# Performance work log

Measured on AMD Instinct MI355X. Metric: run time of the kernel, lower is better.

Reference implementation:

```python
import jax, jax.numpy as jnp
import numpy as np

N = 50000      # nodes
E = 800000     # edges
D = 128        # in = out features (required by Euler residual update)
GRID_SIZE = 5
K = 3          # spline order
GRID_LO, GRID_HI = -1.0, 1.0
EPSILON = 0.001
NUM_BASES = GRID_SIZE + K  # 8


def make_grid(in_features):
    # extended uniform grid: [in, grid_size + 2k + 1]
    h = (GRID_HI - GRID_LO) / GRID_SIZE
    g = jnp.arange(-K, GRID_SIZE + K + 1, dtype=jnp.float32) * h + GRID_LO
    return jnp.broadcast_to(g, (in_features, g.shape[0]))


def b_splines(x, grid):
    # x: [N, in]; grid: [in, g+2k+1] -> bases: [N, in, g+k] (Cox-de Boor)
    xe = x[..., None]
    bases = ((xe >= grid[:, :-1]) & (xe < grid[:, 1:])).astype(x.dtype)
    for j in range(1, K + 1):
        left = (xe - grid[:, : -(j + 1)]) / (grid[:, j:-1] - grid[:, : -(j + 1)])
        right = (grid[:, j + 1:] - xe) / (grid[:, j + 1:] - grid[:, 1:-j])
        bases = left * bases[..., :-1] + right * bases[..., 1:]
    return bases


def kan_transform(x, base_w, spline_w, grid):
    # efficient-KAN layer (scale_and_bias=False): silu base branch + spline branch
    base = jax.nn.silu(x) @ base_w.T                    # [N, out]
    sb = b_splines(x, grid)                             # [N, in, g+k]
    spl = jnp.einsum('nib,oib->no', sb, spline_w)       # [N, out]
    return base + spl


def gcn_norm_coeffs(edge_index, n):
    # A_hat symmetric normalization: deg includes self-loop (+1)
    src, dst = edge_index[0], edge_index[1]
    deg = jnp.zeros((n,), jnp.float32).at[dst].add(1.0) + 1.0
    dis = jax.lax.rsqrt(deg)
    return dis[src] * dis[dst]


def setup_inputs() -> dict:
    key = jax.random.key(0)
    ks = jax.random.split(key, 6)
    x = jax.random.uniform(ks[0], (N, D), jnp.float32) * 2.0 - 1.0  # in grid_range
    edge_index = jax.random.randint(ks[1], (2, E), 0, N, dtype=jnp.int64)
    base_w_l = jax.random.normal(ks[2], (D, D), jnp.float32) * (1.0 / np.sqrt(D))
    spline_w_l = jax.random.normal(ks[3], (D, D, NUM_BASES), jnp.float32) * 0.1
    base_w_c = jax.random.normal(ks[4], (D, D), jnp.float32) * (1.0 / np.sqrt(D))
    spline_w_c = jax.random.normal(ks[5], (D, D, NUM_BASES), jnp.float32) * 0.1
    return {"x": x, "edge_index": edge_index, "base_w_l": base_w_l,
            "spline_w_l": spline_w_l, "base_w_c": base_w_c,
            "spline_w_c": spline_w_c, "delta_t": 2}


def reference(x, edge_index, base_w_l, spline_w_l, base_w_c, spline_w_c, delta_t):
    grid = make_grid(D)
    src, dst = edge_index[0], edge_index[1]
    norm = gcn_norm_coeffs(edge_index, N)  # [E]

    def layer(h):
        # KANLayer branch on node features
        h_l = kan_transform(h, base_w_l, spline_w_l, grid)
        # KANConv branch: aggregate_first -> normalized scatter-add, then KAN
        msgs = norm[:, None] * h[src]                              # [E, D]
        agg = jax.ops.segment_sum(msgs, dst, num_segments=N)       # [N, D]
        h_c = kan_transform(agg, base_w_c, spline_w_c, grid)
        return h_l + h_c

    for _ in range(int(delta_t)):   # explicit Euler ODE steps
        x = x + EPSILON * layer(x)
    return x
```

## Files before the change

### kernel.cpp

```cpp
#include <hip/hip_runtime.h>
#include <hip/hip_bf16.h>

#define NNODES 50000
#define NEDGES 800000
#define DF 128
#define KW 1152
#define EPS 0.001f
#define NB 196

typedef __bf16 bf16x8 __attribute__((ext_vector_type(8)));
typedef __bf16 bf16x4 __attribute__((ext_vector_type(4)));
typedef float  f32x4  __attribute__((ext_vector_type(4)));
typedef unsigned long ulongx2 __attribute__((ext_vector_type(2)));

__global__ void build_wt(const float* __restrict__ bwl, const float* __restrict__ swl,
                         const float* __restrict__ bwc, const float* __restrict__ swc,
                         __bf16* __restrict__ wtf) {
    int idx = blockIdx.x * 256 + threadIdx.x;
    int j    = idx & 7;
    int lane = (idx >> 3) & 63;
    int nj   = (idx >> 9) & 7;
    int t    = idx >> 12;
    int l15 = lane & 15, q = lane >> 4;
    int bc = (t >= 36);
    int ck = bc ? t - 36 : t;
    const float* bw = bc ? bwc : bwl;
    const float* sw = bc ? swc : swl;
    int row = nj * 16 + l15;
    int k = ck * 32 + q * 8 + j;
    float v = (k < 128) ? bw[row * DF + k] : sw[row * 1024 + (k - 128)];
    wtf[idx] = (__bf16)v;
}

__global__ void cast_x(const float* __restrict__ x, __bf16* __restrict__ xb) {
    int i = blockIdx.x * 256 + threadIdx.x;
    f32x4 a = ((const f32x4*)x)[2 * i];
    f32x4 b = ((const f32x4*)x)[2 * i + 1];
    bf16x8 o;
    o[0] = (__bf16)a[0]; o[1] = (__bf16)a[1]; o[2] = (__bf16)a[2]; o[3] = (__bf16)a[3];
    o[4] = (__bf16)b[0]; o[5] = (__bf16)b[1]; o[6] = (__bf16)b[2]; o[7] = (__bf16)b[3];
    ((bf16x8*)xb)[i] = o;
}

__global__ void deg_count(const int* __restrict__ ei, int* __restrict__ deg) {
    int e = blockIdx.x * 256 + threadIdx.x;
    if (e >= NEDGES) return;
    atomicAdd(&deg[ei[NEDGES + e]], 1);
}

__global__ void scan_part(const int* __restrict__ deg, int* __restrict__ bsum) {
    __shared__ int red[256];
    int t = threadIdx.x;
    int i = blockIdx.x * 256 + t;
    red[t] = (i < NNODES) ? deg[i] : 0;
    __syncthreads();
    for (int off = 128; off > 0; off >>= 1) {
        if (t < off) red[t] += red[t + off];
        __syncthreads();
    }
    if (t == 0) bsum[blockIdx.x] = red[0];
}

__global__ void scan_bsum(const int* __restrict__ bsum, int* __restrict__ boff) {
    __shared__ int buf[256];
    int t = threadIdx.x;
    int v = (t < NB) ? bsum[t] : 0;
    buf[t] = v;
    __syncthreads();
    for (int off = 1; off < 256; off <<= 1) {
        int x = (t >= off) ? buf[t - off] : 0;
        __syncthreads();
        buf[t] += x;
        __syncthreads();
    }
    if (t <= NB) boff[t] = buf[t] - ((t < NB) ? bsum[t] : 0);
}

__global__ void scan_final(const int* __restrict__ deg, const int* __restrict__ boff,
                           int* __restrict__ rowptr) {
    __shared__ int buf[256];
    int t = threadIdx.x;
    int i = blockIdx.x * 256 + t;
    int v = (i < NNODES) ? deg[i] : 0;
    buf[t] = v;
    __syncthreads();
    for (int off = 1; off < 256; off <<= 1) {
        int x = (t >= off) ? buf[t - off] : 0;
        __syncthreads();
        buf[t] += x;
        __syncthreads();
    }
    if (i < NNODES) rowptr[i] = buf[t] - v + boff[blockIdx.x];
    if (blockIdx.x == 0 && t == 0) rowptr[NNODES] = boff[NB];
}

__global__ void fill_csr(const int* __restrict__ ei, const int* __restrict__ deg,
                         const int* __restrict__ rowptr, int* __restrict__ cnt,
                         int* __restrict__ esrc, float* __restrict__ ew) {
    int e = blockIdx.x * 256 + threadIdx.x;
    if (e >= NEDGES) return;
    int s = ei[e];
    int d = ei[NEDGES + e];
    float w = rsqrtf((float)(deg[s] + 1)) * rsqrtf((float)(deg[d] + 1));
    int p = rowptr[d] + atomicAdd(&cnt[d], 1);
    esrc[p] = s;
    ew[p] = w;
}

__global__ __launch_bounds__(256) void agg_gather(
        const int* __restrict__ rowptr, const int* __restrict__ esrc,
        const float* __restrict__ ew, const __bf16* __restrict__ hb,
        __bf16* __restrict__ aggb) {
    const int tid = blockIdx.x * 256 + threadIdx.x;
    const int n = tid >> 4;
    const int l = tid & 15;
    if (n >= NNODES) return;
    int p  = rowptr[n];
    const int pe = rowptr[n + 1];
    float acc[8] = {};
    int   cs0, cs1, cs2, cs3;
    float cw0, cw1, cw2, cw3;
    bool have = (p + 3 < pe);
    if (have) {
        cs0 = esrc[p]; cs1 = esrc[p + 1]; cs2 = esrc[p + 2]; cs3 = esrc[p + 3];
        cw0 = ew[p];   cw1 = ew[p + 1];   cw2 = ew[p + 2];   cw3 = ew[p + 3];
    }
    while (have) {
        int np = p + 4;
        bool nh = (np + 3 < pe);
        int   ns0 = 0, ns1 = 0, ns2 = 0, ns3 = 0;
        float nw0 = 0, nw1 = 0, nw2 = 0, nw3 = 0;
        if (nh) {
            ns0 = esrc[np]; ns1 = esrc[np + 1]; ns2 = esrc[np + 2]; ns3 = esrc[np + 3];
            nw0 = ew[np];   nw1 = ew[np + 1];   nw2 = ew[np + 2];   nw3 = ew[np + 3];
        }
        bf16x8 v0 = *(const bf16x8*)(hb + (size_t)cs0 * DF + l * 8);
        bf16x8 v1 = *(const bf16x8*)(hb + (size_t)cs1 * DF + l * 8);
        bf16x8 v2 = *(const bf16x8*)(hb + (size_t)cs2 * DF + l * 8);
        bf16x8 v3 = *(const bf16x8*)(hb + (size_t)cs3 * DF + l * 8);
#pragma unroll
        for (int j = 0; j < 8; ++j)
            acc[j] += cw0 * (float)v0[j] + cw1 * (float)v1[j]
                    + cw2 * (float)v2[j] + cw3 * (float)v3[j];
        p = np;
        cs0 = ns0; cs1 = ns1; cs2 = ns2; cs3 = ns3;
        cw0 = nw0; cw1 = nw1; cw2 = nw2; cw3 = nw3;
        have = nh;
    }
    for (; p < pe; ++p) {
        int   s0 = esrc[p];
        float w0 = ew[p];
        bf16x8 v0 = *(const bf16x8*)(hb + (size_t)s0 * DF + l * 8);
#pragma unroll
        for (int j = 0; j < 8; ++j) acc[j] += w0 * (float)v0[j];
    }
    bf16x8 o;
#pragma unroll
    for (int j = 0; j < 8; ++j) o[j] = (__bf16)acc[j];
    *(bf16x8*)(aggb + (size_t)n * DF + l * 8) = o;
}

__global__ __launch_bounds__(256, 3) void kan_step(
        const float* __restrict__ h,
        const __bf16* __restrict__ xb,
        const __bf16* __restrict__ aggb,
        const __bf16* __restrict__ wtf,
        float* __restrict__ out, __bf16* __restrict__ outb) {
    __shared__ __bf16 Xs[64 * 128];

    const int tid  = threadIdx.x;
    const int lane = tid & 63;
    const int w    = tid >> 6;
    const int q    = lane >> 4, l15 = lane & 15;
    const int n0   = blockIdx.x * 64;
    const int myrow = w * 16 + l15;
    const int msw   = myrow & 7;

    const int xrow = tid >> 2, xseg = tid & 3;
    const bool xok = (n0 + xrow) < NNODES;
    const size_t xgoff = (size_t)(n0 + xrow) * DF + xseg * 32;

    const __bf16* fbase = wtf + (size_t)lane * 8;

    f32x4 acc[8] = {};

    auto xs_write = [&](uint4 v0, uint4 v1, uint4 v2, uint4 v3) {
        const int gl = xrow * 16 + xseg * 4;
        const int sw = xrow & 7;
        *(uint4*)&Xs[(size_t)((gl + 0) ^ sw) * 8] = v0;
        *(uint4*)&Xs[(size_t)((gl + 1) ^ sw) * 8] = v1;
        *(uint4*)&Xs[(size_t)((gl + 2) ^ sw) * 8] = v2;
        *(uint4*)&Xs[(size_t)((gl + 3) ^ sw) * 8] = v3;
    };

    auto loadF = [&](bf16x8 (&bX)[8], int t) {
        const __bf16* fb = fbase + (size_t)t * 4096;
#pragma unroll
        for (int nj = 0; nj < 8; ++nj)
            bX[nj] = *(const bf16x8*)(fb + nj * 512);
    };

    auto spline_pack = [&](float x) -> bf16x8 {
        float f  = __builtin_fmaf(x, 2.5f, 5.5f);
        float fi = floorf(f);
        int  idx = (int)fi;
        float u  = f - fi;
        float u2 = u * u, u3 = u2 * u;
        float om = 1.0f - u;
        float Wa = u3 * (1.0f / 6.0f);
        float Wb = (((-3.0f * u + 3.0f) * u + 3.0f) * u + 1.0f) * (1.0f / 6.0f);
        float Wc = ((3.0f * u - 6.0f) * u2 + 4.0f) * (1.0f / 6.0f);
        float Wd = om * om * om * (1.0f / 6.0f);
        unsigned long p =
              (unsigned long)__builtin_bit_cast(unsigned short, (__bf16)Wd)
            | ((unsigned long)__builtin_bit_cast(unsigned short, (__bf16)Wc) << 16)
            | ((unsigned long)__builtin_bit_cast(unsigned short, (__bf16)Wb) << 32)
            | ((unsigned long)__builtin_bit_cast(unsigned short, (__bf16)Wa) << 48);
        int tt = idx - 3;
        unsigned long lo, hi;
        if (tt >= 0) {
            int s = (tt & 3) * 16;
            unsigned long sv = p << s;
            unsigned long cr = (p >> (63 - s)) >> 1;
            bool hh = tt >= 4;
            lo = hh ? 0ul : sv;
            hi = hh ? sv : cr;
            if (tt >= 8) { lo = 0; hi = 0; }
        } else {
            int s = (-tt) * 16;
            lo = (tt >= -3) ? (p >> (s & 63)) : 0ul;
            hi = 0;
        }
        ulongx2 r; r[0] = lo; r[1] = hi;
        return __builtin_bit_cast(bf16x8, r);
    };

    auto silu8 = [&](const __bf16* xs) -> bf16x8 {
        bf16x8 v = *(const bf16x8*)xs;
        bf16x8 o;
#pragma unroll
        for (int j = 0; j < 8; ++j) {
            float x = (float)v[j];
            o[j] = (__bf16)(x / (1.0f + __expf(-x)));
        }
        return o;
    };

    auto compute = [&](int t, const bf16x8 (&bF)[8]) {
        const int ck = (t >= 36) ? t - 36 : t;
        bf16x8 a;
        if (ck < 4) {
            const int g = (myrow * 16 + ck * 4 + q) ^ msw;
            a = silu8(&Xs[(size_t)g * 8]);
        } else {
            const int f = (ck - 4) * 4 + q;
            const int g = (myrow * 16 + (f >> 3)) ^ msw;
            unsigned short u0 =
                *(const unsigned short*)&Xs[(size_t)g * 8 + (f & 7)];
            a = spline_pack(__builtin_bit_cast(float, (unsigned)u0 << 16));
        }
#pragma unroll
        for (int nj = 0; nj < 8; ++nj)
            acc[nj] = __builtin_amdgcn_mfma_f32_16x16x32_bf16(a, bF[nj], acc[nj], 0, 0, 0);
    };

    uint4 a0 = {}, a1 = {}, a2 = {}, a3 = {};
    uint4 c0 = {}, c1 = {}, c2 = {}, c3 = {};
    if (xok) {
        const uint4* ga = (const uint4*)(xb + xgoff);
        a0 = ga[0]; a1 = ga[1]; a2 = ga[2]; a3 = ga[3];
        const uint4* gc = (const uint4*)(aggb + xgoff);
        c0 = gc[0]; c1 = gc[1]; c2 = gc[2]; c3 = gc[3];
    }
    xs_write(a0, a1, a2, a3);
    asm volatile("s_waitcnt lgkmcnt(0)" ::: "memory");

    bf16x8 bA[8], bB[8];
    loadF(bA, 0);
    loadF(bB, 1);

    for (int t = 0; t < 70; t += 2) {
        if (t == 36) {
            xs_write(c0, c1, c2, c3);
            asm volatile("s_waitcnt lgkmcnt(0)" ::: "memory");
        }
        compute(t, bA);
        loadF(bA, t + 2);
        compute(t + 1, bB);
        if (t + 3 < 72) loadF(bB, t + 3);
    }
    compute(70, bA);
    compute(71, bB);

#pragma unroll
    for (int nj = 0; nj < 8; ++nj) {
#pragma unroll
        for (int r = 0; r < 4; ++r) {
            int row = n0 + w * 16 + q * 4 + r;
            int col = nj * 16 + l15;
            if (row < NNODES) {
                size_t idx = (size_t)row * DF + col;
                float v = h[idx] + EPS * acc[nj][r];
                out[idx]  = v;
                outb[idx] = (__bf16)v;
            }
        }
    }
}

extern "C" void kernel_launch(void* const* d_in, const int* in_sizes, int n_in,
                              void* d_out, int out_size, void* d_ws, size_t ws_size,
                              hipStream_t stream) {
    const float* x   = (const float*)d_in[0];
    const int*   ei  = (const int*)d_in[1];
    const float* bwl = (const float*)d_in[2];
    const float* swl = (const float*)d_in[3];
    const float* bwc = (const float*)d_in[4];
    const float* swc = (const float*)d_in[5];
    float* out = (float*)d_out;

    char* ws = (char*)d_ws;
    int*    deg    = (int*)  (ws + 0);
    int*    cnt    = (int*)  (ws + 200000);
    int*    rowptr = (int*)  (ws + 400000);
    int*    bsum   = (int*)  (ws + 600064);
    int*    boff   = (int*)  (ws + 600896);
    int*    esrc   = (int*)  (ws + 601728);
    float*  ew     = (float*)(ws + 3801728);
    __bf16* xb     = (__bf16*)(ws + 7001728);
    __bf16* aggb   = (__bf16*)(ws + 19801728);
    __bf16* wtf    = (__bf16*)(ws + 32601728);

    build_wt<<<1152, 256, 0, stream>>>(bwl, swl, bwc, swc, wtf);
    cast_x<<<3125, 256, 0, stream>>>(x, xb);

    hipMemsetAsync(deg, 0, 400000, stream);
    deg_count<<<3125, 256, 0, stream>>>(ei, deg);
    scan_part<<<NB, 256, 0, stream>>>(deg, bsum);
    scan_bsum<<<1, 256, 0, stream>>>(bsum, boff);
    scan_final<<<NB, 256, 0, stream>>>(deg, boff, rowptr);
    fill_csr<<<3125, 256, 0, stream>>>(ei, deg, rowptr, cnt, esrc, ew);

    const int gemm_grid = (NNODES + 63) / 64;
    const float* h = x;
    for (int step = 0; step < 2; ++step) {
        agg_gather<<<3125, 256, 0, stream>>>(rowptr, esrc, ew, xb, aggb);
        kan_step<<<gemm_grid, 256, 0, stream>>>(h, xb, aggb, wtf, out, xb);
        h = out;
    }
}
```

Baseline: 414.6 us.

## Co-schedule KAN-layer GEMM with aggregation gather in one heterogeneous launch

Splits the fused KAN step so the KANLayer branch (depends only on x) runs in the same grid as the sparse aggregation gather, interleaving one GEMM block per four gather blocks. The intent is to overlap the memory-bound gather with the MFMA-bound KANLayer work, leaving only the conv branch in the second kernel. The cost is an extra bf16 partial-result buffer written and reread, which adds rounding of the layer branch and extra traffic. The combined kernel also shares one launch bound, which may cap occupancy for the gather blocks.

```diff
diff --git a/kernel.cpp b/kernel.cpp
--- a/kernel.cpp
+++ b/kernel.cpp
@@ -4,12 +4,10 @@
 #define NNODES 50000
 #define NEDGES 800000
 #define DF 128
-#define KW 1152
 #define EPS 0.001f
 #define NB 196
 
 typedef __bf16 bf16x8 __attribute__((ext_vector_type(8)));
-typedef __bf16 bf16x4 __attribute__((ext_vector_type(4)));
 typedef float  f32x4  __attribute__((ext_vector_type(4)));
 typedef unsigned long ulongx2 __attribute__((ext_vector_type(2)));
 
@@ -107,64 +105,197 @@
     ew[p] = w;
 }
 
-__global__ __launch_bounds__(256) void agg_gather(
+__device__ __forceinline__ bf16x8 spline_pack(float x) {
+    float f  = __builtin_fmaf(x, 2.5f, 5.5f);
+    float fi = floorf(f);
+    int  idx = (int)fi;
+    float u  = f - fi;
+    float u2 = u * u, u3 = u2 * u;
+    float om = 1.0f - u;
+    float Wa = u3 * (1.0f / 6.0f);
+    float Wb = (((-3.0f * u + 3.0f) * u + 3.0f) * u + 1.0f) * (1.0f / 6.0f);
+    float Wc = ((3.0f * u - 6.0f) * u2 + 4.0f) * (1.0f / 6.0f);
+    float Wd = om * om * om * (1.0f / 6.0f);
+    unsigned long p =
+          (unsigned long)__builtin_bit_cast(unsigned short, (__bf16)Wd)
+        | ((unsigned long)__builtin_bit_cast(unsigned short, (__bf16)Wc) << 16)
+        | ((unsigned long)__builtin_bit_cast(unsigned short, (__bf16)Wb) << 32)
+        | ((unsigned long)__builtin_bit_cast(unsigned short, (__bf16)Wa) << 48);
+    int tt = idx - 3;
+    unsigned long lo, hi;
+    if (tt >= 0) {
+        int s = (tt & 3) * 16;
+        unsigned long sv = p << s;
+        unsigned long cr = (p >> (63 - s)) >> 1;
+        bool hh = tt >= 4;
+        lo = hh ? 0ul : sv;
+        hi = hh ? sv : cr;
+        if (tt >= 8) { lo = 0; hi = 0; }
+    } else {
+        int s = (-tt) * 16;
+        lo = (tt >= -3) ? (p >> (s & 63)) : 0ul;
+        hi = 0;
+    }
+    ulongx2 r; r[0] = lo; r[1] = hi;
+    return __builtin_bit_cast(bf16x8, r);
+}
+
+__device__ __forceinline__ bf16x8 silu8v(bf16x8 v) {
+    bf16x8 o;
+#pragma unroll
+    for (int j = 0; j < 8; ++j) {
+        float x = (float)v[j];
+        o[j] = (__bf16)(x / (1.0f + __expf(-x)));
+    }
+    return o;
+}
+
+__global__ __launch_bounds__(256, 4) void agg_kanl(
         const int* __restrict__ rowptr, const int* __restrict__ esrc,
-        const float* __restrict__ ew, const __bf16* __restrict__ hb,
-        __bf16* __restrict__ aggb) {
-    const int tid = blockIdx.x * 256 + threadIdx.x;
-    const int n = tid >> 4;
-    const int l = tid & 15;
-    if (n >= NNODES) return;
-    int p  = rowptr[n];
-    const int pe = rowptr[n + 1];
-    float acc[8] = {};
-    int   cs0, cs1, cs2, cs3;
-    float cw0, cw1, cw2, cw3;
-    bool have = (p + 3 < pe);
-    if (have) {
-        cs0 = esrc[p]; cs1 = esrc[p + 1]; cs2 = esrc[p + 2]; cs3 = esrc[p + 3];
-        cw0 = ew[p];   cw1 = ew[p + 1];   cw2 = ew[p + 2];   cw3 = ew[p + 3];
-    }
-    while (have) {
-        int np = p + 4;
-        bool nh = (np + 3 < pe);
-        int   ns0 = 0, ns1 = 0, ns2 = 0, ns3 = 0;
-        float nw0 = 0, nw1 = 0, nw2 = 0, nw3 = 0;
-        if (nh) {
-            ns0 = esrc[np]; ns1 = esrc[np + 1]; ns2 = esrc[np + 2]; ns3 = esrc[np + 3];
-            nw0 = ew[np];   nw1 = ew[np + 1];   nw2 = ew[np + 2];   nw3 = ew[np + 3];
-        }
-        bf16x8 v0 = *(const bf16x8*)(hb + (size_t)cs0 * DF + l * 8);
-        bf16x8 v1 = *(const bf16x8*)(hb + (size_t)cs1 * DF + l * 8);
-        bf16x8 v2 = *(const bf16x8*)(hb + (size_t)cs2 * DF + l * 8);
-        bf16x8 v3 = *(const bf16x8*)(hb + (size_t)cs3 * DF + l * 8);
-#pragma unroll
-        for (int j = 0; j < 8; ++j)
-            acc[j] += cw0 * (float)v0[j] + cw1 * (float)v1[j]
-                    + cw2 * (float)v2[j] + cw3 * (float)v3[j];
-        p = np;
-        cs0 = ns0; cs1 = ns1; cs2 = ns2; cs3 = ns3;
-        cw0 = nw0; cw1 = nw1; cw2 = nw2; cw3 = nw3;
-        have = nh;
-    }
-    for (; p < pe; ++p) {
-        int   s0 = esrc[p];
-        float w0 = ew[p];
-        bf16x8 v0 = *(const bf16x8*)(hb + (size_t)s0 * DF + l * 8);
-#pragma unroll
-        for (int j = 0; j < 8; ++j) acc[j] += w0 * (float)v0[j];
-    }
-    bf16x8 o;
-#pragma unroll
-    for (int j = 0; j < 8; ++j) o[j] = (__bf16)acc[j];
-    *(bf16x8*)(aggb + (size_t)n * DF + l * 8) = o;
-}
-
-__global__ __launch_bounds__(256, 3) void kan_step(
+        const float* __restrict__ ew, const __bf16* __restrict__ xb,
+        __bf16* __restrict__ aggb, const __bf16* __restrict__ wtf,
+        __bf16* __restrict__ accb) {
+    __shared__ __bf16 Xs[64 * 128];
+
+    const int bid = blockIdx.x;
+    const int k5 = bid / 5, r5 = bid - k5 * 5;
+    const bool isKanl = (r5 == 4) || (bid == 3906);
+
+    if (!isKanl) {
+        const int ablk = k5 * 4 + r5;
+        const int vtid = ablk * 256 + threadIdx.x;
+        const int n = vtid >> 4;
+        const int l = vtid & 15;
+        if (n >= NNODES) return;
+        int p  = rowptr[n];
+        const int pe = rowptr[n + 1];
+        float acc[8] = {};
+        int   cs0, cs1, cs2, cs3;
+        float cw0, cw1, cw2, cw3;
+        bool have = (p + 3 < pe);
+        if (have) {
+            cs0 = esrc[p]; cs1 = esrc[p + 1]; cs2 = esrc[p + 2]; cs3 = esrc[p + 3];
+            cw0 = ew[p];   cw1 = ew[p + 1];   cw2 = ew[p + 2];   cw3 = ew[p + 3];
+        }
+        while (have) {
+            int np = p + 4;
+            bool nh = (np + 3 < pe);
+            int   ns0 = 0, ns1 = 0, ns2 = 0, ns3 = 0;
+            float nw0 = 0, nw1 = 0, nw2 = 0, nw3 = 0;
+            if (nh) {
+                ns0 = esrc[np]; ns1 = esrc[np + 1]; ns2 = esrc[np + 2]; ns3 = esrc[np + 3];
+                nw0 = ew[np];   nw1 = ew[np + 1];   nw2 = ew[np + 2];   nw3 = ew[np + 3];
+            }
+            bf16x8 v0 = *(const bf16x8*)(xb + (size_t)cs0 * DF + l * 8);
+            bf16x8 v1 = *(const bf16x8*)(xb + (size_t)cs1 * DF + l * 8);
+            bf16x8 v2 = *(const bf16x8*)(xb + (size_t)cs2 * DF + l * 8);
+            bf16x8 v3 = *(const bf16x8*)(xb + (size_t)cs3 * DF + l * 8);
+#pragma unroll
+            for (int j = 0; j < 8; ++j)
+                acc[j] += cw0 * (float)v0[j] + cw1 * (float)v1[j]
+                        + cw2 * (float)v2[j] + cw3 * (float)v3[j];
+            p = np;
+            cs0 = ns0; cs1 = ns1; cs2 = ns2; cs3 = ns3;
+            cw0 = nw0; cw1 = nw1; cw2 = nw2; cw3 = nw3;
+            have = nh;
+        }
+        for (; p < pe; ++p) {
+            int   s0 = esrc[p];
+            float w0 = ew[p];
+            bf16x8 v0 = *(const bf16x8*)(xb + (size_t)s0 * DF + l * 8);
+#pragma unroll
+            for (int j = 0; j < 8; ++j) acc[j] += w0 * (float)v0[j];
+        }
+        bf16x8 o;
+#pragma unroll
+        for (int j = 0; j < 8; ++j) o[j] = (__bf16)acc[j];
+        *(bf16x8*)(aggb + (size_t)n * DF + l * 8) = o;
+        return;
+    }
+
+    const int kblk = (bid == 3906) ? 781 : k5;
+    const int tid  = threadIdx.x;
+    const int lane = tid & 63;
+    const int w    = tid >> 6;
+    const int q    = lane >> 4, l15 = lane & 15;
+    const int n0   = kblk * 64;
+    const int myrow = w * 16 + l15;
+    const int msw   = myrow & 7;
+
+    const int xrow = tid >> 2, xseg = tid & 3;
+    const bool xok = (n0 + xrow) < NNODES;
+    const size_t xgoff = (size_t)(n0 + xrow) * DF + xseg * 32;
+
+    const __bf16* fbase = wtf + (size_t)lane * 8;
+
+    f32x4 acc[8] = {};
+
+    {
+        uint4 a0 = {}, a1 = {}, a2 = {}, a3 = {};
+        if (xok) {
+            const uint4* ga = (const uint4*)(xb + xgoff);
+            a0 = ga[0]; a1 = ga[1]; a2 = ga[2]; a3 = ga[3];
+        }
+        const int gl = xrow * 16 + xseg * 4;
+        const int sw = xrow & 7;
+        *(uint4*)&Xs[(size_t)((gl + 0) ^ sw) * 8] = a0;
+        *(uint4*)&Xs[(size_t)((gl + 1) ^ sw) * 8] = a1;
+        *(uint4*)&Xs[(size_t)((gl + 2) ^ sw) * 8] = a2;
+        *(uint4*)&Xs[(size_t)((gl + 3) ^ sw) * 8] = a3;
+    }
+    asm volatile("s_waitcnt lgkmcnt(0)" ::: "memory");
+
+    auto loadF = [&](bf16x8 (&bX)[8], int t) {
+        const __bf16* fb = fbase + (size_t)t * 4096;
+#pragma unroll
+        for (int nj = 0; nj < 8; ++nj)
+            bX[nj] = *(const bf16x8*)(fb + nj * 512);
+    };
+    auto compute = [&](int ck, const bf16x8 (&bF)[8]) {
+        bf16x8 a;
+        if (ck < 4) {
+            const int g = (myrow * 16 + ck * 4 + q) ^ msw;
+            a = silu8v(*(const bf16x8*)&Xs[(size_t)g * 8]);
+        } else {
+            const int f = (ck - 4) * 4 + q;
+            const int g = (myrow * 16 + (f >> 3)) ^ msw;
+            unsigned short u0 = *(const unsigned short*)&Xs[(size_t)g * 8 + (f & 7)];
+            a = spline_pack(__builtin_bit_cast(float, (unsigned)u0 << 16));
+        }
+#pragma unroll
+        for (int nj = 0; nj < 8; ++nj)
+            acc[nj] = __builtin_amdgcn_mfma_f32_16x16x32_bf16(a, bF[nj], acc[nj], 0, 0, 0);
+    };
+
+    bf16x8 bA[8], bB[8];
+    loadF(bA, 0);
+    loadF(bB, 1);
+    for (int t = 0; t < 34; t += 2) {
+        compute(t, bA);
+        loadF(bA, t + 2);
+        compute(t + 1, bB);
+        if (t + 3 < 36) loadF(bB, t + 3);
+    }
+    compute(34, bA);
+    compute(35, bB);
+
+#pragma unroll
+    for (int nj = 0; nj < 8; ++nj) {
+#pragma unroll
+        for (int r = 0; r < 4; ++r) {
+            int row = n0 + w * 16 + q * 4 + r;
+            int col = nj * 16 + l15;
+            if (row < NNODES)
+                accb[(size_t)row * DF + col] = (__bf16)acc[nj][r];
+        }
+    }
+}
+
+__global__ __launch_bounds__(256, 3) void kan_c(
         const float* __restrict__ h,
-        const __bf16* __restrict__ xb,
         const __bf16* __restrict__ aggb,
         const __bf16* __restrict__ wtf,
+        const __bf16* __restrict__ accb,
         float* __restrict__ out, __bf16* __restrict__ outb) {
     __shared__ __bf16 Xs[64 * 128];
 
@@ -180,83 +311,40 @@
     const bool xok = (n0 + xrow) < NNODES;
     const size_t xgoff = (size_t)(n0 + xrow) * DF + xseg * 32;
 
-    const __bf16* fbase = wtf + (size_t)lane * 8;
+    const __bf16* fbase = wtf + (size_t)36 * 4096 + (size_t)lane * 8;
 
     f32x4 acc[8] = {};
 
-    auto xs_write = [&](uint4 v0, uint4 v1, uint4 v2, uint4 v3) {
+    {
+        uint4 a0 = {}, a1 = {}, a2 = {}, a3 = {};
+        if (xok) {
+            const uint4* ga = (const uint4*)(aggb + xgoff);
+            a0 = ga[0]; a1 = ga[1]; a2 = ga[2]; a3 = ga[3];
+        }
         const int gl = xrow * 16 + xseg * 4;
         const int sw = xrow & 7;
-        *(uint4*)&Xs[(size_t)((gl + 0) ^ sw) * 8] = v0;
-        *(uint4*)&Xs[(size_t)((gl + 1) ^ sw) * 8] = v1;
-        *(uint4*)&Xs[(size_t)((gl + 2) ^ sw) * 8] = v2;
-        *(uint4*)&Xs[(size_t)((gl + 3) ^ sw) * 8] = v3;
-    };
-
-    auto loadF = [&](bf16x8 (&bX)[8], int t) {
-        const __bf16* fb = fbase + (size_t)t * 4096;
+        *(uint4*)&Xs[(size_t)((gl + 0) ^ sw) * 8] = a0;
+        *(uint4*)&Xs[(size_t)((gl + 1) ^ sw) * 8] = a1;
+        *(uint4*)&Xs[(size_t)((gl + 2) ^ sw) * 8] = a2;
+        *(uint4*)&Xs[(size_t)((gl + 3) ^ sw) * 8] = a3;
+    }
+    asm volatile("s_waitcnt lgkmcnt(0)" ::: "memory");
+
+    auto loadF = [&](bf16x8 (&bX)[8], int u) {
+        const __bf16* fb = fbase + (size_t)u * 4096;
 #pragma unroll
         for (int nj = 0; nj < 8; ++nj)
             bX[nj] = *(const bf16x8*)(fb + nj * 512);
     };
-
-    auto spline_pack = [&](float x) -> bf16x8 {
-        float f  = __builtin_fmaf(x, 2.5f, 5.5f);
-        float fi = floorf(f);
-        int  idx = (int)fi;
-        float u  = f - fi;
-        float u2 = u * u, u3 = u2 * u;
-        float om = 1.0f - u;
-        float Wa = u3 * (1.0f / 6.0f);
-        float Wb = (((-3.0f * u + 3.0f) * u + 3.0f) * u + 1.0f) * (1.0f / 6.0f);
-        float Wc = ((3.0f * u - 6.0f) * u2 + 4.0f) * (1.0f / 6.0f);
-        float Wd = om * om * om * (1.0f / 6.0f);
-        unsigned long p =
-              (unsigned long)__builtin_bit_cast(unsigned short, (__bf16)Wd)
-            | ((unsigned long)__builtin_bit_cast(unsigned short, (__bf16)Wc) << 16)
-            | ((unsigned long)__builtin_bit_cast(unsigned short, (__bf16)Wb) << 32)
-            | ((unsigned long)__builtin_bit_cast(unsigned short, (__bf16)Wa) << 48);
-        int tt = idx - 3;
-        unsigned long lo, hi;
-        if (tt >= 0) {
-            int s = (tt & 3) * 16;
-            unsigned long sv = p << s;
-            unsigned long cr = (p >> (63 - s)) >> 1;
-            bool hh = tt >= 4;
-            lo = hh ? 0ul : sv;
-            hi = hh ? sv : cr;
-            if (tt >= 8) { lo = 0; hi = 0; }
-        } else {
-            int s = (-tt) * 16;
-            lo = (tt >= -3) ? (p >> (s & 63)) : 0ul;
-            hi = 0;
-        }
-        ulongx2 r; r[0] = lo; r[1] = hi;
-        return __builtin_bit_cast(bf16x8, r);
-    };
-
-    auto silu8 = [&](const __bf16* xs) -> bf16x8 {
-        bf16x8 v = *(const bf16x8*)xs;
-        bf16x8 o;
-#pragma unroll
-        for (int j = 0; j < 8; ++j) {
-            float x = (float)v[j];
-            o[j] = (__bf16)(x / (1.0f + __expf(-x)));
-        }
-        return o;
-    };
-
-    auto compute = [&](int t, const bf16x8 (&bF)[8]) {
-        const int ck = (t >= 36) ? t - 36 : t;
+    auto compute = [&](int ck, const bf16x8 (&bF)[8]) {
         bf16x8 a;
         if (ck < 4) {
             const int g = (myrow * 16 + ck * 4 + q) ^ msw;
-            a = silu8(&Xs[(size_t)g * 8]);
+            a = silu8v(*(const bf16x8*)&Xs[(size_t)g * 8]);
         } else {
             const int f = (ck - 4) * 4 + q;
             const int g = (myrow * 16 + (f >> 3)) ^ msw;
-            unsigned short u0 =
-                *(const unsigned short*)&Xs[(size_t)g * 8 + (f & 7)];
+            unsigned short u0 = *(const unsigned short*)&Xs[(size_t)g * 8 + (f & 7)];
             a = spline_pack(__builtin_bit_cast(float, (unsigned)u0 << 16));
         }
 #pragma unroll
@@ -264,33 +352,17 @@
             acc[nj] = __builtin_amdgcn_mfma_f32_16x16x32_bf16(a, bF[nj], acc[nj], 0, 0, 0);
     };
 
-    uint4 a0 = {}, a1 = {}, a2 = {}, a3 = {};
-    uint4 c0 = {}, c1 = {}, c2 = {}, c3 = {};
-    if (xok) {
-        const uint4* ga = (const uint4*)(xb + xgoff);
-        a0 = ga[0]; a1 = ga[1]; a2 = ga[2]; a3 = ga[3];
-        const uint4* gc = (const uint4*)(aggb + xgoff);
-        c0 = gc[0]; c1 = gc[1]; c2 = gc[2]; c3 = gc[3];
-    }
-    xs_write(a0, a1, a2, a3);
-    asm volatile("s_waitcnt lgkmcnt(0)" ::: "memory");
-
     bf16x8 bA[8], bB[8];
     loadF(bA, 0);
     loadF(bB, 1);
-
-    for (int t = 0; t < 70; t += 2) {
-        if (t == 36) {
-            xs_write(c0, c1, c2, c3);
-            asm volatile("s_waitcnt lgkmcnt(0)" ::: "memory");
-        }
-        compute(t, bA);
-        loadF(bA, t + 2);
-        compute(t + 1, bB);
-        if (t + 3 < 72) loadF(bB, t + 3);
-    }
-    compute(70, bA);
-    compute(71, bB);
+    for (int u = 0; u < 34; u += 2) {
+        compute(u, bA);
+        loadF(bA, u + 2);
+        compute(u + 1, bB);
+        if (u + 3 < 36) loadF(bB, u + 3);
+    }
+    compute(34, bA);
+    compute(35, bB);
 
 #pragma unroll
     for (int nj = 0; nj < 8; ++nj) {
@@ -300,7 +372,7 @@
             int col = nj * 16 + l15;
             if (row < NNODES) {
                 size_t idx = (size_t)row * DF + col;
-                float v = h[idx] + EPS * acc[nj][r];
+                float v = h[idx] + EPS * (acc[nj][r] + (float)accb[idx]);
                 out[idx]  = v;
                 outb[idx] = (__bf16)v;
             }
@@ -330,22 +402,22 @@
     __bf16* xb     = (__bf16*)(ws + 7001728);
     __bf16* aggb   = (__bf16*)(ws + 19801728);
     __bf16* wtf    = (__bf16*)(ws + 32601728);
+    __bf16* accb   = (__bf16*)(ws + 33191552);
 
     build_wt<<<1152, 256, 0, stream>>>(bwl, swl, bwc, swc, wtf);
     cast_x<<<3125, 256, 0, stream>>>(x, xb);
 
-    hipMemsetAsync(deg, 0, 400000, stream);
+    (void)hipMemsetAsync(deg, 0, 400000, stream);
     deg_count<<<3125, 256, 0, stream>>>(ei, deg);
     scan_part<<<NB, 256, 0, stream>>>(deg, bsum);
     scan_bsum<<<1, 256, 0, stream>>>(bsum, boff);
     scan_final<<<NB, 256, 0, stream>>>(deg, boff, rowptr);
     fill_csr<<<3125, 256, 0, stream>>>(ei, deg, rowptr, cnt, esrc, ew);
 
-    const int gemm_grid = (NNODES + 63) / 64;
     const float* h = x;
     for (int step = 0; step < 2; ++step) {
-        agg_gather<<<3125, 256, 0, stream>>>(rowptr, esrc, ew, xb, aggb);
-        kan_step<<<gemm_grid, 256, 0, stream>>>(h, xb, aggb, wtf, out, xb);
+        agg_kanl<<<3907, 256, 0, stream>>>(rowptr, esrc, ew, xb, aggb, wtf, accb);
+        kan_c<<<782, 256, 0, stream>>>(h, aggb, wtf, accb, out, xb);
         h = out;
     }
 }
```

After: 418.9 us. About the same (+1.0%).
